# Kernel tuning notes

Hardware: AMD Instinct MI355X
Metric: run time of the kernel (lower is better)

## Reference

```python
import jax, jax.numpy as jnp
import numpy as np
import math

# Constants from module defaults
NUM_HEADS = 16
STEEP = 10.0        # SpikeFunction surrogate steepness
LEAK = 0.9          # LIF leak_rate
THRESH = 1.0        # spike_threshold
REFRAC = 2.0        # refractory_period
TH_DECAY = 0.95     # adaptive threshold decay

@jax.custom_vjp
def spike_fn(v, th):
    return (v >= th).astype(v.dtype)

def _spike_fwd(v, th):
    return spike_fn(v, th), (v, th)

def _spike_bwd(res, g):
    v, th = res
    s = jax.nn.sigmoid(STEEP * (v - th))
    return (g * STEEP * s * (1.0 - s), jnp.zeros_like(th))

spike_fn.defvjp(_spike_fwd, _spike_bwd)


def lif(cur_seq, W_rec, theta):
    """Leaky integrate-and-fire recurrence.
    cur_seq: [S, N, Dh] precomputed input currents (input_weights applied already).
    Returns spikes [S, N, Dh]."""
    S, N, Dh = cur_seq.shape
    dt = cur_seq.dtype
    init = (jnp.zeros((N, Dh), dt),               # membrane potential
            jnp.zeros((N, Dh), dt),               # spike history (detached)
            jnp.zeros((N, Dh), dt),               # refractory counter
            jnp.full((N, Dh), THRESH, dt))        # adaptive threshold

    def step(state, cur):
        v, hist, refrac, athr = state
        total = cur + hist @ W_rec.T
        v = LEAK * v + total
        v = v * (refrac <= 0).astype(dt)          # refractory masking
        spikes = spike_fn(v, athr)
        sm = jax.lax.stop_gradient(spikes)        # spike_mask (bool in torch, no grad)
        v = v * (1.0 - sm)                        # membrane reset
        refrac = jnp.maximum(refrac - 1.0, sm * REFRAC)
        athr = TH_DECAY * athr + sm * theta       # adaptive threshold bump
        return (v, sm, refrac, athr), spikes

    _, spikes = jax.lax.scan(step, init, cur_seq)
    return spikes


def setup_inputs() -> dict:
    key = jax.random.key(0)
    B, S, D = 4, 1024, 1024
    H = NUM_HEADS
    Dh = D // H
    ks = jax.random.split(key, 16)
    sD = 1.0 / math.sqrt(D)
    sd = 1.0 / math.sqrt(Dh)
    inp = {
        "x": jax.random.normal(ks[0], (B, S, D), jnp.float32),
        "Wq": jax.random.normal(ks[1], (D, D), jnp.float32) * sD,
        "Wk": jax.random.normal(ks[2], (D, D), jnp.float32) * sD,
        "Wv": jax.random.normal(ks[3], (D, D), jnp.float32) * sD,
        "Wo": jax.random.normal(ks[4], (D, D), jnp.float32) * sD,
        "bo": jax.random.normal(ks[5], (D,), jnp.float32) * sD,
        "Wq_in": jax.random.normal(ks[6], (Dh, Dh), jnp.float32) * sd,
        "Wq_rec": jax.random.normal(ks[7], (Dh, Dh), jnp.float32) * sd,
        "Wk_in": jax.random.normal(ks[8], (Dh, Dh), jnp.float32) * sd,
        "Wk_rec": jax.random.normal(ks[9], (Dh, Dh), jnp.float32) * sd,
        "Wv_in": jax.random.normal(ks[10], (Dh, Dh), jnp.float32) * sd,
        "Wv_rec": jax.random.normal(ks[11], (Dh, Dh), jnp.float32) * sd,
        "theta_q": jnp.full((Dh,), 0.1, jnp.float32),
        "theta_k": jnp.full((Dh,), 0.1, jnp.float32),
        "theta_v": jnp.full((Dh,), 0.1, jnp.float32),
    }
    return inp


def reference(x, Wq, Wk, Wv, Wo, bo, Wq_in, Wq_rec, Wk_in, Wk_rec,
              Wv_in, Wv_rec, theta_q, theta_k, theta_v):
    B, S, D = x.shape
    H = NUM_HEADS
    Dh = D // H

    def heads_time_major(t):
        # [B,S,D] -> [S, B*H, Dh]
        return t.reshape(B, S, H, Dh).transpose(1, 0, 2, 3).reshape(S, B * H, Dh)

    # Projections; LIF input current is linear so apply input_weights over whole seq
    cur_q = heads_time_major(x @ Wq.T) @ Wq_in.T
    cur_k = heads_time_major(x @ Wk.T) @ Wk_in.T
    cur_v = heads_time_major(x @ Wv.T) @ Wv_in.T

    qs = lif(cur_q, Wq_rec, theta_q)
    ks_ = lif(cur_k, Wk_rec, theta_k)
    vs = lif(cur_v, Wv_rec, theta_v)

    def back(t):
        # [S, B*H, Dh] -> [B, H, S, Dh]
        return t.reshape(S, B, H, Dh).transpose(1, 2, 0, 3)

    qh, kh, vh = back(qs), back(ks_), back(vs)
    scale = 1.0 / math.sqrt(Dh)
    scores = jnp.einsum('bhqd,bhkd->bhqk', qh, kh) * scale
    attn = jax.nn.softmax(scores, axis=-1)
    ctx = jnp.einsum('bhqk,bhkd->bhqd', attn, vh)
    out = ctx.transpose(0, 2, 1, 3).reshape(B, S, D) @ Wo.T + bo
    return out
```

## Files before the change

### kernel.cpp

```cpp
#include <hip/hip_runtime.h>
#include <hip/hip_bf16.h>

#define B_  4
#define S_  1024
#define D_  1024
#define H_  16
#define DH_ 64
#define N_  64
#define BS_ 4096

#define WS_CUR   0ull
#define WS_XH    (WS_CUR + 48ull*1024*1024)
#define WS_XL    (WS_XH  +  8ull*1024*1024)
#define WS_WCH   (WS_XL  +  8ull*1024*1024)
#define WS_WCL   (WS_WCH +  6ull*1024*1024)
#define WS_MSK   (WS_WCL +  6ull*1024*1024)
#define WS_CTXH  WS_XH
#define WS_CTXL  WS_XL
#define WS_WOH   WS_WCH
#define WS_WOL   (WS_WCH + 2ull*1024*1024)

typedef __attribute__((ext_vector_type(8))) short short8v;
typedef __attribute__((ext_vector_type(4))) float f32x4;

__device__ inline void bsplit(float x, unsigned short& h, unsigned short& l) {
    unsigned ux = __float_as_uint(x);
    unsigned rh = (ux + 0x7FFFu + ((ux >> 16) & 1u)) >> 16;
    h = (unsigned short)rh;
    float r = x - __uint_as_float(rh << 16);
    unsigned ur = __float_as_uint(r);
    l = (unsigned short)((ur + 0x7FFFu + ((ur >> 16) & 1u)) >> 16);
}

__global__ __launch_bounds__(256) void k_split_x(
    const float* __restrict__ x, unsigned short* __restrict__ xh, unsigned short* __restrict__ xl)
{
    int i = (blockIdx.x * 256 + threadIdx.x) * 4;
    float4 v = *reinterpret_cast<const float4*>(&x[i]);
    ushort4 h, l;
    bsplit(v.x, h.x, l.x);
    bsplit(v.y, h.y, l.y);
    bsplit(v.z, h.z, l.z);
    bsplit(v.w, h.w, l.w);
    *reinterpret_cast<ushort4*>(&xh[i]) = h;
    *reinterpret_cast<ushort4*>(&xl[i]) = l;
}

__global__ __launch_bounds__(256) void k_wc_split(
    const float* __restrict__ Wq, const float* __restrict__ Wk, const float* __restrict__ Wv,
    const float* __restrict__ Wqi, const float* __restrict__ Wki, const float* __restrict__ Wvi,
    unsigned short* __restrict__ wch, unsigned short* __restrict__ wcl)
{
    int z = blockIdx.y, hd = blockIdx.x;
    const float* W  = (z == 0) ? Wq  : (z == 1) ? Wk  : Wv;
    const float* Wi = (z == 0) ? Wqi : (z == 1) ? Wki : Wvi;
    int h = hd >> 6, d = hd & 63;
    int tid = threadIdx.x;

    __shared__ float ws[64];
    if (tid < 64) ws[tid] = Wi[d * 64 + tid];
    __syncthreads();

    const float* Wb = W + (size_t)h * 64 * 1024;
    float acc[4] = {0.f, 0.f, 0.f, 0.f};
    for (int j = 0; j < 64; j++) {
        float wv = ws[j];
        const float* row = Wb + (size_t)j * 1024;
        #pragma unroll
        for (int mi = 0; mi < 4; mi++)
            acc[mi] += row[tid + mi * 256] * wv;
    }
    unsigned short* oh = wch + (size_t)z * 1024 * 1024 + (size_t)hd * 1024;
    unsigned short* ol = wcl + (size_t)z * 1024 * 1024 + (size_t)hd * 1024;
    #pragma unroll
    for (int mi = 0; mi < 4; mi++) {
        unsigned short hh, ll;
        bsplit(acc[mi], hh, ll);
        oh[tid + mi * 256] = hh;
        ol[tid + mi * 256] = ll;
    }
}

__global__ __launch_bounds__(256) void k_split_wo(
    const float* __restrict__ Wo, unsigned short* __restrict__ wh, unsigned short* __restrict__ wl)
{
    int i = (blockIdx.x * 256 + threadIdx.x) * 4;
    float4 v = *reinterpret_cast<const float4*>(&Wo[i]);
    ushort4 h, l;
    bsplit(v.x, h.x, l.x);
    bsplit(v.y, h.y, l.y);
    bsplit(v.z, h.z, l.z);
    bsplit(v.w, h.w, l.w);
    *reinterpret_cast<ushort4*>(&wh[i]) = h;
    *reinterpret_cast<ushort4*>(&wl[i]) = l;
}

template<int OUT>
__global__ __launch_bounds__(512, 4) void k_mfma_gemm(
    const unsigned short* __restrict__ Ah, const unsigned short* __restrict__ Al,
    const unsigned short* __restrict__ Bh, const unsigned short* __restrict__ Bl,
    float* __restrict__ C, const float* __restrict__ bias)
{
    __shared__ __align__(16) unsigned short lds[4 * 128 * 64];

    int tid = threadIdx.x;
    int bx = blockIdx.x, by = blockIdx.y, bz = blockIdx.z;
    const unsigned short* Bhz = Bh + (size_t)bz * 1024 * 1024;
    const unsigned short* Blz = Bl + (size_t)bz * 1024 * 1024;
    int rb = bx * 128, cb = by * 128;

    int wid = tid >> 6, lane = tid & 63;
    int wr = wid >> 2, wc = wid & 3;
    int r15 = lane & 15, g = lane >> 4;

    int rowA = lane >> 3;
    int kpsw = ((lane & 7) ^ rowA) * 8;

    f32x4 acc[4][2];
    #pragma unroll
    for (int mt = 0; mt < 4; mt++)
        #pragma unroll
        for (int nt = 0; nt < 2; nt++)
            acc[mt][nt] = (f32x4){0.f, 0.f, 0.f, 0.f};

    #pragma unroll 1
    for (int t = 0; t < 16; t++) {
        int kb = t * 64;
        #pragma unroll
        for (int i = 0; i < 8; i++) {
            int q = wid * 8 + i;
            int mat = q >> 4, ch = q & 15;
            const unsigned short* gsrc = (mat == 0) ? Ah : (mat == 1) ? Al
                                        : (mat == 2) ? Bhz : Blz;
            int rowoff = (mat < 2) ? rb : cb;
            int row = ch * 8 + rowA;
            __builtin_amdgcn_global_load_lds(
                (const __attribute__((address_space(1))) void*)
                    (gsrc + (size_t)(rowoff + row) * 1024 + kb + kpsw),
                (__attribute__((address_space(3))) void*)(&lds[mat * 8192 + ch * 512]),
                16, 0, 0);
        }
        __syncthreads();

        #pragma unroll
        for (int kk = 0; kk < 2; kk++) {
            short8v bh[2], bl[2];
            #pragma unroll
            for (int nt = 0; nt < 2; nt++) {
                int Crow = wc * 32 + nt * 16 + r15;
                int off = Crow * 64 + (((kk * 4 + g) ^ (Crow & 7)) * 8);
                bh[nt] = *reinterpret_cast<const short8v*>(&lds[2 * 8192 + off]);
                bl[nt] = *reinterpret_cast<const short8v*>(&lds[3 * 8192 + off]);
            }
            #pragma unroll
            for (int mt = 0; mt < 4; mt++) {
                int Arow = wr * 64 + mt * 16 + r15;
                int off = Arow * 64 + (((kk * 4 + g) ^ (Arow & 7)) * 8);
                short8v ah = *reinterpret_cast<const short8v*>(&lds[0 * 8192 + off]);
                short8v al = *reinterpret_cast<const short8v*>(&lds[1 * 8192 + off]);
                #pragma unroll
                for (int nt = 0; nt < 2; nt++) {
                    acc[mt][nt] = __builtin_amdgcn_mfma_f32_16x16x32_bf16(bh[nt], ah, acc[mt][nt], 0, 0, 0);
                    acc[mt][nt] = __builtin_amdgcn_mfma_f32_16x16x32_bf16(bl[nt], ah, acc[mt][nt], 0, 0, 0);
                    acc[mt][nt] = __builtin_amdgcn_mfma_f32_16x16x32_bf16(bh[nt], al, acc[mt][nt], 0, 0, 0);
                }
            }
        }
        __syncthreads();
    }

    if (OUT == 0) {
        float* out = C + (size_t)bz * 64 * 1024 * 64;
        int b = rb >> 10;
        #pragma unroll
        for (int nt = 0; nt < 2; nt++) {
            int col = cb + wc * 32 + nt * 16 + g * 4;
            int h = col >> 6, dd = col & 63;
            #pragma unroll
            for (int mt = 0; mt < 4; mt++) {
                int row = rb + wr * 64 + mt * 16 + r15;
                int s = row & 1023;
                f32x4 a = acc[mt][nt];
                *reinterpret_cast<float4*>(&out[(((size_t)(b * 16 + h)) * 1024 + s) * 64 + dd]) =
                    make_float4(a[0], a[1], a[2], a[3]);
            }
        }
    } else {
        #pragma unroll
        for (int nt = 0; nt < 2; nt++) {
            int col = cb + wc * 32 + nt * 16 + g * 4;
            float4 bv = *reinterpret_cast<const float4*>(&bias[col]);
            #pragma unroll
            for (int mt = 0; mt < 4; mt++) {
                int row = rb + wr * 64 + mt * 16 + r15;
                f32x4 a = acc[mt][nt];
                *reinterpret_cast<float4*>(&C[(size_t)row * 1024 + col]) =
                    make_float4(a[0] + bv.x, a[1] + bv.y, a[2] + bv.z, a[3] + bv.w);
            }
        }
    }
}

__global__ __launch_bounds__(64) void k_lif(
    const float* __restrict__ curAll,
    const float* __restrict__ Wrq, const float* __restrict__ Wrk, const float* __restrict__ Wrv,
    const float* __restrict__ thq, const float* __restrict__ thk, const float* __restrict__ thv,
    unsigned long long* __restrict__ masks)
{
    __shared__ float T[16 * 16 * 64];
    __shared__ __align__(16) float cbuf[2][64 * 64];

    int bid = blockIdx.x;
    int l = bid >> 6, n = bid & 63;
    const float* W  = (l == 0) ? Wrq : (l == 1) ? Wrk : Wrv;
    const float* th = (l == 0) ? thq : (l == 1) ? thk : thv;
    const float* cbase = curAll + (((size_t)l * 64 + n) * 1024) * 64;
    unsigned long long* mout = masks + ((size_t)l * 64 + n) * 1024;
    int d = threadIdx.x;

    #pragma unroll
    for (int j = 0; j < 16; j++)
        __builtin_amdgcn_global_load_lds(
            (const __attribute__((address_space(1))) void*)(cbase + j * 256 + d * 4),
            (__attribute__((address_space(3))) void*)(&cbuf[0][j * 256]), 16, 0, 0);

    float theta = th[d];

    for (int g = 0; g < 16; g++) {
        float w0 = W[d * 64 + 4 * g + 0];
        float w1 = W[d * 64 + 4 * g + 1];
        float w2 = W[d * 64 + 4 * g + 2];
        float w3 = W[d * 64 + 4 * g + 3];
        #pragma unroll
        for (int c = 0; c < 16; c++) {
            float t = 0.f;
            if (c & 1) t += w0;
            if (c & 2) t += w1;
            if (c & 4) t += w2;
            if (c & 8) t += w3;
            T[g * 1024 + c * 64 + d] = t;
        }
    }
    __syncthreads();

    float v = 0.f, refrac = 0.f, athr = 1.0f;
    unsigned mlo = 0u, mhi = 0u;
    unsigned bufLo = 0u, bufHi = 0u;

    for (int b = 0; b < 16; b++) {
        if (b < 15) {
            const float* src = cbase + (size_t)(b + 1) * 4096;
            float* dst = cbuf[(b + 1) & 1];
            #pragma unroll
            for (int j = 0; j < 16; j++)
                __builtin_amdgcn_global_load_lds(
                    (const __attribute__((address_space(1))) void*)(src + j * 256 + d * 4),
                    (__attribute__((address_space(3))) void*)(dst + j * 256), 16, 0, 0);
        }
        if (b == 0)      asm volatile("s_waitcnt vmcnt(16)" ::: "memory");
        else if (b < 15) asm volatile("s_waitcnt vmcnt(17)" ::: "memory");
        else             asm volatile("s_waitcnt vmcnt(0)"  ::: "memory");

        const float* cb = cbuf[b & 1];
        #pragma unroll 8
        for (int i = 0; i < 64; i++) {
            float curv = cb[i * 64 + d];

            float t[16];
            #pragma unroll
            for (int g = 0; g < 8; g++)
                t[g] = T[g * 1024 + (int)(((mlo >> (4 * g)) & 15u) << 6) + d];
            #pragma unroll
            for (int g = 0; g < 8; g++)
                t[8 + g] = T[(8 + g) * 1024 + (int)(((mhi >> (4 * g)) & 15u) << 6) + d];

            #pragma unroll
            for (int k = 8; k >= 1; k >>= 1)
                #pragma unroll
                for (int j = 0; j < k; j++)
                    t[j] = t[j] + t[j + k];
            float total = curv + t[0];

            v = 0.9f * v + total;
            v = (refrac <= 0.f) ? v : 0.f;
            bool sp = (v >= athr);
            unsigned long long m = __ballot(sp);
            mlo = (unsigned)m;
            mhi = (unsigned)(m >> 32);
            bufLo = (d == i) ? mlo : bufLo;
            bufHi = (d == i) ? mhi : bufHi;
            float sm = sp ? 1.f : 0.f;
            v = sp ? 0.f : v;
            refrac = fmaxf(refrac - 1.f, sm * 2.f);
            athr = 0.95f * athr + sm * theta;
        }
        mout[b * 64 + d] = ((unsigned long long)bufHi << 32) | bufLo;
    }
}

#define ATT_C1 0.180336879f
#define ATT_C2 11.541560327f

__device__ inline short8v expand8(unsigned byte) {
    short8v r;
    #pragma unroll
    for (int e = 0; e < 8; e++)
        r[e] = (short)(((byte >> e) & 1u) ? 0x3F80 : 0);
    return r;
}

__device__ inline unsigned bfpk(float x, float y) {
    unsigned ux = __float_as_uint(x);
    unsigned uy = __float_as_uint(y);
    unsigned rx = (ux + 0x7FFFu + ((ux >> 16) & 1u)) >> 16;
    unsigned ry = (uy + 0x7FFFu + ((uy >> 16) & 1u)) >> 16;
    return rx | (ry << 16);
}

__global__ __launch_bounds__(256) void k_attn_mfma(
    const unsigned long long* __restrict__ masks,
    unsigned short* __restrict__ ctxh, unsigned short* __restrict__ ctxl)
{
    __shared__ __align__(16) unsigned short Klds[128][72];
    __shared__ __align__(16) unsigned short Vt[64][136];
    __shared__ unsigned long long vmbuf[2][128];

    const unsigned long long* qm_all = masks;
    const unsigned long long* km_all = masks + (size_t)64 * 1024;
    const unsigned long long* vm_all = masks + (size_t)2 * 64 * 1024;

    int n  = blockIdx.y;
    int qc = blockIdx.x;
    int tid = threadIdx.x;
    int wv = tid >> 6;
    int lane = tid & 63;
    int r15 = lane & 15, g = lane >> 4;

    const unsigned long long* km = km_all + (size_t)n * 1024;
    const unsigned long long* vm = vm_all + (size_t)n * 1024;

    unsigned long long qmask = qm_all[(size_t)n * 1024 + qc * 64 + wv * 16 + r15];
    short8v Qf[2];
    #pragma unroll
    for (int ch = 0; ch < 2; ch++)
        Qf[ch] = expand8((unsigned)(qmask >> ((ch * 4 + g) * 8)) & 0xFFu);

    f32x4 cx[4];
    #pragma unroll
    for (int mt = 0; mt < 4; mt++) cx[mt] = (f32x4){0.f, 0.f, 0.f, 0.f};
    float den = 0.f;

    if (tid < 128) vmbuf[0][tid] = vm[tid];
    __syncthreads();

    for (int kt = 0; kt < 8; kt++) {
        {
            int s = tid >> 1, half = tid & 1;
            unsigned long long m = km[kt * 128 + s];
            #pragma unroll
            for (int j = 0; j < 4; j++) {
                unsigned byte = (unsigned)(m >> (half * 32 + j * 8)) & 0xFFu;
                *reinterpret_cast<short8v*>(&Klds[s][(half * 4 + j) * 8]) = expand8(byte);
            }
        }
        {
            int dh = tid & 63;
            int sc4 = tid >> 6;
            #pragma unroll
            for (int j = 0; j < 4; j++) {
                short8v v2;
                #pragma unroll
                for (int e = 0; e < 8; e++) {
                    unsigned long long mv = vmbuf[kt & 1][sc4 * 32 + j * 8 + e];
                    v2[e] = (short)(((mv >> dh) & 1ull) ? 0x3F80 : 0);
                }
                *reinterpret_cast<short8v*>(&Vt[dh][(sc4 * 4 + j) * 8]) = v2;
            }
        }
        __syncthreads();

        if (tid < 128 && kt + 1 < 8) vmbuf[(kt + 1) & 1][tid] = vm[(kt + 1) * 128 + tid];

        f32x4 pf[8];
        #pragma unroll
        for (int mt = 0; mt < 8; mt++) {
            f32x4 c = (f32x4){0.f, 0.f, 0.f, 0.f};
            #pragma unroll
            for (int ch = 0; ch < 2; ch++) {
                short8v a = *reinterpret_cast<const short8v*>(&Klds[mt * 16 + r15][(ch * 4 + g) * 8]);
                c = __builtin_amdgcn_mfma_f32_16x16x32_bf16(a, Qf[ch], c, 0, 0, 0);
            }
            f32x4 p;
            #pragma unroll
            for (int i = 0; i < 4; i++) {
                p[i] = exp2f(c[i] * ATT_C1 - ATT_C2);
                den += p[i];
            }
            pf[mt] = p;
        }

        int src0 = ((g & 1) << 1) * 16 + r15;
        int src1 = src0 + 16;
        bool hi = (g >= 2);
        #pragma unroll
        for (int c4 = 0; c4 < 4; c4++) {
            unsigned d0 = bfpk(pf[2 * c4][0], pf[2 * c4][1]);
            unsigned d1 = bfpk(pf[2 * c4][2], pf[2 * c4][3]);
            unsigned d2 = bfpk(pf[2 * c4 + 1][0], pf[2 * c4 + 1][1]);
            unsigned d3 = bfpk(pf[2 * c4 + 1][2], pf[2 * c4 + 1][3]);
            unsigned a0 = __shfl((int)d0, src0), b0 = __shfl((int)d2, src0);
            unsigned a1 = __shfl((int)d1, src0), b1 = __shfl((int)d3, src0);
            unsigned a2 = __shfl((int)d0, src1), b2 = __shfl((int)d2, src1);
            unsigned a3 = __shfl((int)d1, src1), b3 = __shfl((int)d3, src1);
            union { unsigned u[4]; short8v s; } bw;
            bw.u[0] = hi ? b0 : a0;
            bw.u[1] = hi ? b1 : a1;
            bw.u[2] = hi ? b2 : a2;
            bw.u[3] = hi ? b3 : a3;
            #pragma unroll
            for (int mt = 0; mt < 4; mt++) {
                short8v a = *reinterpret_cast<const short8v*>(&Vt[mt * 16 + r15][(c4 * 4 + g) * 8]);
                cx[mt] = __builtin_amdgcn_mfma_f32_16x16x32_bf16(a, bw.s, cx[mt], 0, 0, 0);
            }
        }
        __syncthreads();
    }

    den += __shfl_xor(den, 16);
    den += __shfl_xor(den, 32);
    float inv = 1.f / den;

    int b = n >> 4, h = n & 15;
    int row = b * 1024 + qc * 64 + wv * 16 + r15;
    unsigned short* oph = ctxh + (size_t)row * 1024 + h * 64;
    unsigned short* opl = ctxl + (size_t)row * 1024 + h * 64;
    #pragma unroll
    for (int mt = 0; mt < 4; mt++)
        #pragma unroll
        for (int i = 0; i < 4; i++) {
            unsigned short hh, ll;
            bsplit(cx[mt][i] * inv, hh, ll);
            oph[mt * 16 + g * 4 + i] = hh;
            opl[mt * 16 + g * 4 + i] = ll;
        }
}

extern "C" void kernel_launch(void* const* d_in, const int* in_sizes, int n_in,
                              void* d_out, int out_size, void* d_ws, size_t ws_size,
                              hipStream_t stream) {
    const float* x    = (const float*)d_in[0];
    const float* Wq   = (const float*)d_in[1];
    const float* Wk   = (const float*)d_in[2];
    const float* Wv   = (const float*)d_in[3];
    const float* Wo   = (const float*)d_in[4];
    const float* bo   = (const float*)d_in[5];
    const float* Wqi  = (const float*)d_in[6];
    const float* Wqr  = (const float*)d_in[7];
    const float* Wki  = (const float*)d_in[8];
    const float* Wkr  = (const float*)d_in[9];
    const float* Wvi  = (const float*)d_in[10];
    const float* Wvr  = (const float*)d_in[11];
    const float* thq  = (const float*)d_in[12];
    const float* thk  = (const float*)d_in[13];
    const float* thv  = (const float*)d_in[14];

    char* ws = (char*)d_ws;
    float* cur = (float*)(ws + WS_CUR);
    unsigned short* xh  = (unsigned short*)(ws + WS_XH);
    unsigned short* xl  = (unsigned short*)(ws + WS_XL);
    unsigned short* wch = (unsigned short*)(ws + WS_WCH);
    unsigned short* wcl = (unsigned short*)(ws + WS_WCL);
    unsigned long long* masks = (unsigned long long*)(ws + WS_MSK);
    unsigned short* ctxh = (unsigned short*)(ws + WS_CTXH);
    unsigned short* ctxl = (unsigned short*)(ws + WS_CTXL);
    unsigned short* woh = (unsigned short*)(ws + WS_WOH);
    unsigned short* wol = (unsigned short*)(ws + WS_WOL);
    float* outp = (float*)d_out;

    k_split_x<<<dim3(4096, 1, 1), 256, 0, stream>>>(x, xh, xl);
    k_wc_split<<<dim3(1024, 3, 1), 256, 0, stream>>>(Wq, Wk, Wv, Wqi, Wki, Wvi, wch, wcl);
    k_mfma_gemm<0><<<dim3(32, 8, 3), 512, 0, stream>>>(xh, xl, wch, wcl, cur, nullptr);
    k_split_wo<<<dim3(1024, 1, 1), 256, 0, stream>>>(Wo, woh, wol);
    k_lif<<<dim3(192, 1, 1), 64, 0, stream>>>(cur, Wqr, Wkr, Wvr, thq, thk, thv, masks);
    k_attn_mfma<<<dim3(16, 64, 1), 256, 0, stream>>>(masks, ctxh, ctxl);
    k_mfma_gemm<1><<<dim3(32, 8, 1), 512, 0, stream>>>(ctxh, ctxl, woh, wol, outp, bo);
}
```

Measured before the change: 414.6 us.

## Compute LIF recurrent matvec with bf16 split MFMA instead of LDS lookup tables

Replaces the per-step 4-bit lookup-table gather from LDS (16 LDS reads plus an add tree per timestep) with MFMA 16x16x32 bf16 matrix ops. The weights live in registers as hi/lo bf16 pairs for near-fp32 accuracy, and the spike mask is expanded into the A operand. It also skips the matvec entirely when the previous spike mask is zero. This removes the table build, the barrier and the LDS pressure, but adds 16 dependent MFMAs per step on the serial recurrence critical path, which costs latency.

```diff
diff --git a/kernel.cpp b/kernel.cpp
--- a/kernel.cpp
+++ b/kernel.cpp
@@ -207,7 +207,6 @@
     const float* __restrict__ thq, const float* __restrict__ thk, const float* __restrict__ thv,
     unsigned long long* __restrict__ masks)
 {
-    __shared__ float T[16 * 16 * 64];
     __shared__ __align__(16) float cbuf[2][64 * 64];
 
     int bid = blockIdx.x;
@@ -217,6 +216,29 @@
     const float* cbase = curAll + (((size_t)l * 64 + n) * 1024) * 64;
     unsigned long long* mout = masks + ((size_t)l * 64 + n) * 1024;
     int d = threadIdx.x;
+    int r15 = d & 15, g = d >> 4;
+
+    short8v Wh[4][2], Wl[4][2];
+    #pragma unroll
+    for (int t = 0; t < 4; t++)
+        #pragma unroll
+        for (int c = 0; c < 2; c++) {
+            const float* wr = W + (size_t)(16 * t + r15) * 64 + 32 * c + g * 8;
+            float4 w0 = *reinterpret_cast<const float4*>(wr);
+            float4 w1 = *reinterpret_cast<const float4*>(wr + 4);
+            float wv[8] = {w0.x, w0.y, w0.z, w0.w, w1.x, w1.y, w1.z, w1.w};
+            short8v hi, lo;
+            #pragma unroll
+            for (int e = 0; e < 8; e++) {
+                unsigned short hh, ll;
+                bsplit(wv[e], hh, ll);
+                hi[e] = (short)hh;
+                lo[e] = (short)ll;
+            }
+            Wh[t][c] = hi;
+            Wl[t][c] = lo;
+        }
+    float theta = th[d];
 
     #pragma unroll
     for (int j = 0; j < 16; j++)
@@ -224,28 +246,10 @@
             (const __attribute__((address_space(1))) void*)(cbase + j * 256 + d * 4),
             (__attribute__((address_space(3))) void*)(&cbuf[0][j * 256]), 16, 0, 0);
 
-    float theta = th[d];
-
-    for (int g = 0; g < 16; g++) {
-        float w0 = W[d * 64 + 4 * g + 0];
-        float w1 = W[d * 64 + 4 * g + 1];
-        float w2 = W[d * 64 + 4 * g + 2];
-        float w3 = W[d * 64 + 4 * g + 3];
-        #pragma unroll
-        for (int c = 0; c < 16; c++) {
-            float t = 0.f;
-            if (c & 1) t += w0;
-            if (c & 2) t += w1;
-            if (c & 4) t += w2;
-            if (c & 8) t += w3;
-            T[g * 1024 + c * 64 + d] = t;
-        }
-    }
-    __syncthreads();
-
     float v = 0.f, refrac = 0.f, athr = 1.0f;
-    unsigned mlo = 0u, mhi = 0u;
+    unsigned long long mask = 0ull;
     unsigned bufLo = 0u, bufHi = 0u;
+    const f32x4 zero4 = (f32x4){0.f, 0.f, 0.f, 0.f};
 
     for (int b = 0; b < 16; b++) {
         if (b < 15) {
@@ -261,34 +265,59 @@
         else if (b < 15) asm volatile("s_waitcnt vmcnt(17)" ::: "memory");
         else             asm volatile("s_waitcnt vmcnt(0)"  ::: "memory");
 
-        const float* cb = cbuf[b & 1];
-        #pragma unroll 8
+        const float* cbp = cbuf[b & 1];
+        #pragma unroll 2
         for (int i = 0; i < 64; i++) {
-            float curv = cb[i * 64 + d];
-
-            float t[16];
-            #pragma unroll
-            for (int g = 0; g < 8; g++)
-                t[g] = T[g * 1024 + (int)(((mlo >> (4 * g)) & 15u) << 6) + d];
-            #pragma unroll
-            for (int g = 0; g < 8; g++)
-                t[8 + g] = T[(8 + g) * 1024 + (int)(((mhi >> (4 * g)) & 15u) << 6) + d];
-
-            #pragma unroll
-            for (int k = 8; k >= 1; k >>= 1)
+            float total = cbp[i * 64 + d];
+            if (mask) {
+                short8v A0, A1;
+                unsigned b0 = (unsigned)(mask >> (g * 8)) & 0xFFu;
+                unsigned b1 = (unsigned)(mask >> (32 + g * 8)) & 0xFFu;
                 #pragma unroll
-                for (int j = 0; j < k; j++)
-                    t[j] = t[j] + t[j + k];
-            float total = curv + t[0];
+                for (int e = 0; e < 8; e++) {
+                    A0[e] = (short)(((b0 >> e) & 1u) ? 0x3F80 : 0);
+                    A1[e] = (short)(((b1 >> e) & 1u) ? 0x3F80 : 0);
+                }
+                float tt0, tt1, tt2, tt3;
+                {
+                    f32x4 a1 = __builtin_amdgcn_mfma_f32_16x16x32_bf16(A0, Wh[0][0], zero4, 0, 0, 0);
+                    a1 = __builtin_amdgcn_mfma_f32_16x16x32_bf16(A1, Wh[0][1], a1, 0, 0, 0);
+                    f32x4 a2 = __builtin_amdgcn_mfma_f32_16x16x32_bf16(A0, Wl[0][0], zero4, 0, 0, 0);
+                    a2 = __builtin_amdgcn_mfma_f32_16x16x32_bf16(A1, Wl[0][1], a2, 0, 0, 0);
+                    tt0 = a1[0] + a2[0];
+                }
+                {
+                    f32x4 a1 = __builtin_amdgcn_mfma_f32_16x16x32_bf16(A0, Wh[1][0], zero4, 0, 0, 0);
+                    a1 = __builtin_amdgcn_mfma_f32_16x16x32_bf16(A1, Wh[1][1], a1, 0, 0, 0);
+                    f32x4 a2 = __builtin_amdgcn_mfma_f32_16x16x32_bf16(A0, Wl[1][0], zero4, 0, 0, 0);
+                    a2 = __builtin_amdgcn_mfma_f32_16x16x32_bf16(A1, Wl[1][1], a2, 0, 0, 0);
+                    tt1 = a1[0] + a2[0];
+                }
+                {
+                    f32x4 a1 = __builtin_amdgcn_mfma_f32_16x16x32_bf16(A0, Wh[2][0], zero4, 0, 0, 0);
+                    a1 = __builtin_amdgcn_mfma_f32_16x16x32_bf16(A1, Wh[2][1], a1, 0, 0, 0);
+                    f32x4 a2 = __builtin_amdgcn_mfma_f32_16x16x32_bf16(A0, Wl[2][0], zero4, 0, 0, 0);
+                    a2 = __builtin_amdgcn_mfma_f32_16x16x32_bf16(A1, Wl[2][1], a2, 0, 0, 0);
+                    tt2 = a1[0] + a2[0];
+                }
+                {
+                    f32x4 a1 = __builtin_amdgcn_mfma_f32_16x16x32_bf16(A0, Wh[3][0], zero4, 0, 0, 0);
+                    a1 = __builtin_amdgcn_mfma_f32_16x16x32_bf16(A1, Wh[3][1], a1, 0, 0, 0);
+                    f32x4 a2 = __builtin_amdgcn_mfma_f32_16x16x32_bf16(A0, Wl[3][0], zero4, 0, 0, 0);
+                    a2 = __builtin_amdgcn_mfma_f32_16x16x32_bf16(A1, Wl[3][1], a2, 0, 0, 0);
+                    tt3 = a1[0] + a2[0];
+                }
+                float s01 = (g & 1) ? tt1 : tt0;
+                float s23 = (g & 1) ? tt3 : tt2;
+                total += (g & 2) ? s23 : s01;
+            }
 
             v = 0.9f * v + total;
             v = (refrac <= 0.f) ? v : 0.f;
             bool sp = (v >= athr);
-            unsigned long long m = __ballot(sp);
-            mlo = (unsigned)m;
-            mhi = (unsigned)(m >> 32);
-            bufLo = (d == i) ? mlo : bufLo;
-            bufHi = (d == i) ? mhi : bufHi;
+            mask = __ballot(sp);
+            bufLo = (d == i) ? (unsigned)mask : bufLo;
+            bufHi = (d == i) ? (unsigned)(mask >> 32) : bufHi;
             float sm = sp ? 1.f : 0.f;
             v = sp ? 0.f : v;
             refrac = fmaxf(refrac - 1.f, sm * 2.f);
```

Result: slower. 571.5 us (+37.8%).
